# Performance work log

Measured on AMD Instinct MI355X. Metric: run time of the kernel, lower is better.

## Reference

```python
import jax, jax.numpy as jnp
import numpy as np

HID = 256
IN_DIM = 256
OUT_DIM = 10
L_CYCLES = 6
H_CYCLES = 3
BATCH = 131072
LN_EPS = 1e-5


def _layernorm(v, w, b):
    mu = jnp.mean(v, axis=-1, keepdims=True)
    var = jnp.mean(jnp.square(v - mu), axis=-1, keepdims=True)
    return (v - mu) * jax.lax.rsqrt(var + LN_EPS) * w + b


def setup_inputs() -> dict:
    key = jax.random.key(0)
    ks = jax.random.split(key, 12)
    s = lambda fan_in: 1.0 / np.sqrt(fan_in)
    inp = {
        "x": jax.random.normal(ks[0], (BATCH, IN_DIM), dtype=jnp.float32),
        "W_in": jax.random.uniform(ks[1], (IN_DIM, HID), jnp.float32, -s(IN_DIM), s(IN_DIM)),
        "b_in": jnp.zeros((HID,), jnp.float32),
        "y_init": jax.random.normal(ks[2], (1, HID), dtype=jnp.float32) * 0.02,
        "W_up": jax.random.uniform(ks[3], (HID, 4 * HID), jnp.float32, -s(HID), s(HID)),
        "b_up": jnp.zeros((4 * HID,), jnp.float32),
        "W_down": jax.random.uniform(ks[4], (4 * HID, HID), jnp.float32, -s(4 * HID), s(4 * HID)),
        "b_down": jnp.zeros((HID,), jnp.float32),
        "ln_w": jnp.ones((HID,), jnp.float32),
        "ln_b": jnp.zeros((HID,), jnp.float32),
        "W_comb": jax.random.uniform(ks[5], (2 * HID, HID), jnp.float32, -s(2 * HID), s(2 * HID)),
        "b_comb": jnp.zeros((HID,), jnp.float32),
        "W_yt": jax.random.uniform(ks[6], (HID, HID), jnp.float32, -s(HID), s(HID)),
        "b_yt": jnp.zeros((HID,), jnp.float32),
        "W_head": jax.random.uniform(ks[7], (HID, OUT_DIM), jnp.float32, -s(HID), s(HID)),
        "b_head": jnp.zeros((OUT_DIM,), jnp.float32),
    }
    return inp


def reference(x, W_in, b_in, y_init, W_up, b_up, W_down, b_down, ln_w, ln_b,
              W_comb, b_comb, W_yt, b_yt, W_head, b_head):
    z = x @ W_in + b_in                      # [B, H]
    y = jnp.broadcast_to(y_init, (x.shape[0], HID))
    for _ in range(H_CYCLES):
        for _ in range(L_CYCLES):
            h = jax.nn.gelu(z @ W_up + b_up, approximate=False)
            h = h @ W_down + b_down
            z = _layernorm(z + h, ln_w, ln_b)
        combined = jnp.concatenate([z, y], axis=-1)   # [B, 2H]
        h = jax.nn.gelu(combined @ W_comb + b_comb, approximate=False)
        y = y + h @ W_yt + b_yt
    return y @ W_head + b_head
```

## Files before the change

### kernel.cpp

```cpp
#include <hip/hip_runtime.h>

typedef _Float16 h16;
typedef h16 h16x8 __attribute__((ext_vector_type(8)));
typedef float f32x4 __attribute__((ext_vector_type(4)));

#define MFMA16(a, b, c) __builtin_amdgcn_mfma_f32_16x16x32_f16(a, b, c, 0, 0, 0)

typedef __attribute__((address_space(1))) const char gconst_char;
typedef __attribute__((address_space(3))) char lds_char;
#define GL_LDS16(g, l) __builtin_amdgcn_global_load_lds((gconst_char*)(g), (lds_char*)(l), 16, 0, 0)

#define WIN_CSH   16384
#define WIN_OFF   0
#define WUP_CSH   16384
#define WUP_OFF   131072
#define WDN_CSH   16384
#define WDN_OFF   655360
#define WCOMB_CSH 32768
#define WCOMB_OFF 1179648
#define WYT_CSH   16384
#define WYT_OFF   1441792
#define WHEAD_SZ  8192
#define WHEAD_OFF 1572864
#define ZY_OFF    1581056
#define ZY_BYTES  (131072UL * 512UL * 2UL)

#define L_WUP0 0
#define L_WUP1 16384
#define L_WDN0 32768
#define L_WDN1 49152
#define L_HS   65536
#define L_BUP  76288
#define L_BDN  80384
#define L_LNW  81408
#define L_LNB  82432
#define SMEM_MEGA 83456

#define C_WC0 0
#define C_WC1 32768
#define C_WY0 65536
#define C_WY1 81920
#define C_GS  98304
#define C_BC  109056
#define C_BY  110080
#define SMEM_COMB 111104

#define SMEM_HEAD 8192

#define SLICE_W 42

__device__ __forceinline__ void stage_calls(const char* src, char* dst, int calls, int wave,
                                            int nw, int lane) {
  for (int i = wave; i < calls; i += nw)
    GL_LDS16(src + i * 1024 + lane * 16, dst + i * 1024);
}

__device__ __forceinline__ float gelu_f(float x) {
  float t = x * (1.5957691216f + 0.0713548354f * x * x);
  float e = __expf(-t);
  return x * __builtin_amdgcn_rcpf(1.0f + e);
}

__global__ void prepC_kernel(const float* __restrict__ src, h16* __restrict__ dst,
                             int Nsrc, int CSHh, int tot) {
  for (int d = blockIdx.x * 256 + threadIdx.x; d < tot; d += gridDim.x * 256) {
    int chunk = d / CSHh, r = d % CSHh;
    int frag = r >> 9, lane = (r >> 3) & 63, j = r & 7;
    int kk = frag >> 1, nt = frag & 1, q = lane >> 4, c = lane & 15;
    int k = kk * 32 + q * 8 + j;
    int n = chunk * 32 + nt * 16 + c;
    dst[d] = (h16)src[(long)k * Nsrc + n];
  }
}
__global__ void prepD_kernel(const float* __restrict__ src, h16* __restrict__ dst, int tot) {
  for (int d = blockIdx.x * 256 + threadIdx.x; d < tot; d += gridDim.x * 256) {
    int chunk = d >> 13, r = d & 8191;
    int nt = r >> 9, lane = (r >> 3) & 63, j = r & 7;
    int q = lane >> 4, c = lane & 15;
    int k = chunk * 32 + q * 8 + j;
    dst[d] = (h16)src[(long)k * 256 + nt * 16 + c];
  }
}
__global__ void prepH_kernel(const float* __restrict__ src, h16* __restrict__ dst) {
  for (int d = blockIdx.x * 256 + threadIdx.x; d < 4096; d += gridDim.x * 256) {
    int kk = d >> 9, lane = (d >> 3) & 63, j = d & 7;
    int q = lane >> 4, c = lane & 15;
    int k = kk * 32 + q * 8 + j;
    dst[d] = (h16)((c < 10) ? src[k * 10 + c] : 0.0f);
  }
}

__global__ __launch_bounds__(512, 2) void mega_kernel(
    const float* x, h16* zy,
    const char* __restrict__ winP, const char* __restrict__ wupP, const char* __restrict__ wdnP,
    const float* __restrict__ b_in, const float* __restrict__ b_up,
    const float* __restrict__ b_down, const float* __restrict__ ln_w,
    const float* __restrict__ ln_b, const float* __restrict__ y_init, int first) {
  extern __shared__ char smem[];
  const int tid = threadIdx.x, wave = tid >> 6, lane = tid & 63;
  const int q = lane >> 4, c = lane & 15;
  const int lane16 = lane << 4;
  const long m0 = (long)blockIdx.x * 128 + wave * 16;

  float* bupL = (float*)(smem + L_BUP);
  float* bdnL = (float*)(smem + L_BDN);
  float* lnwL = (float*)(smem + L_LNW);
  float* lnbL = (float*)(smem + L_LNB);
  for (int i = tid; i < 1024; i += 512) bupL[i] = b_up[i];
  if (tid < 256) { bdnL[tid] = b_down[tid]; lnwL[tid] = ln_w[tid]; lnbL[tid] = ln_b[tid]; }

  f32x4 acc2[16];
  h16x8 az[8];
  h16* sl = (h16*)(smem + L_HS + wave * (SLICE_W * 16 * 2));
  const f32x4 vzero = {0.0f, 0.0f, 0.0f, 0.0f};

  if (first) {
#pragma unroll
    for (int kk = 0; kk < 8; ++kk) {
      const float* p = x + (m0 + c) * 256 + kk * 32 + q * 8;
      f32x4 u0 = *(const f32x4*)p;
      f32x4 u1 = *(const f32x4*)(p + 4);
      h16x8 a;
      a[0] = (h16)u0[0]; a[1] = (h16)u0[1]; a[2] = (h16)u0[2]; a[3] = (h16)u0[3];
      a[4] = (h16)u1[0]; a[5] = (h16)u1[1]; a[6] = (h16)u1[2]; a[7] = (h16)u1[3];
      az[kk] = a;
    }
#pragma unroll
    for (int nt = 0; nt < 16; ++nt) acc2[nt] = vzero;

    stage_calls(winP, smem + L_WUP0, 16, wave, 8, lane);
    __syncthreads();
#pragma unroll
    for (int ncI = 0; ncI < 8; ++ncI) {
      if (ncI < 7)
        stage_calls(winP + (ncI + 1) * WIN_CSH, smem + (((ncI + 1) & 1) ? L_WUP1 : L_WUP0),
                    16, wave, 8, lane);
      const char* wb = smem + ((ncI & 1) ? L_WUP1 : L_WUP0);
#pragma unroll
      for (int kk = 0; kk < 8; ++kk)
#pragma unroll
        for (int nt = 0; nt < 2; ++nt) {
          h16x8 b = *(const h16x8*)(wb + ((kk * 2 + nt) << 10) + lane16);
          acc2[ncI * 2 + nt] = MFMA16(az[kk], b, acc2[ncI * 2 + nt]);
        }
      __syncthreads();
    }
#pragma unroll
    for (int nt = 0; nt < 16; ++nt) {
      float bi = b_in[nt * 16 + c];
#pragma unroll
      for (int r = 0; r < 4; ++r) acc2[nt][r] += bi;
    }
#pragma unroll
    for (int kk = 0; kk < 8; ++kk) {
      const float* p = y_init + kk * 32 + q * 8;
      f32x4 u0 = *(const f32x4*)p;
      f32x4 u1 = *(const f32x4*)(p + 4);
      h16x8 a;
      a[0] = (h16)u0[0]; a[1] = (h16)u0[1]; a[2] = (h16)u0[2]; a[3] = (h16)u0[3];
      a[4] = (h16)u1[0]; a[5] = (h16)u1[1]; a[6] = (h16)u1[2]; a[7] = (h16)u1[3];
      *(h16x8*)(zy + (m0 + c) * 512 + 256 + kk * 32 + q * 8) = a;
    }
    stage_calls(wupP, smem + L_WUP0, 16, wave, 8, lane);
    stage_calls(wdnP, smem + L_WDN0, 16, wave, 8, lane);
#pragma unroll
    for (int kk = 0; kk < 8; ++kk) {
#pragma unroll
      for (int n2 = 0; n2 < 2; ++n2)
#pragma unroll
        for (int r = 0; r < 4; ++r)
          sl[(q * 4 + r) * SLICE_W + n2 * 16 + c] = (h16)acc2[kk * 2 + n2][r];
      az[kk] = *(const h16x8*)(sl + c * SLICE_W + q * 8);
    }
  } else {
    stage_calls(wupP, smem + L_WUP0, 16, wave, 8, lane);
    stage_calls(wdnP, smem + L_WDN0, 16, wave, 8, lane);
#pragma unroll
    for (int kk = 0; kk < 8; ++kk)
      az[kk] = *(const h16x8*)(zy + (m0 + c) * 512 + kk * 32 + q * 8);
#pragma unroll
    for (int kk = 0; kk < 8; ++kk) {
      *(h16x8*)(sl + c * SLICE_W + q * 8) = az[kk];
#pragma unroll
      for (int n2 = 0; n2 < 2; ++n2)
#pragma unroll
        for (int r = 0; r < 4; ++r)
          acc2[kk * 2 + n2][r] = (float)sl[(q * 4 + r) * SLICE_W + n2 * 16 + c];
    }
  }

  for (int it = 0; it < 6; ++it) {
    for (int nc = 0; nc < 32; ++nc) {
      const int tc = it * 32 + nc;
      __syncthreads();
      if (tc < 191) {
        const int nxt = (nc + 1) & 31;
        char* wu = smem + (((tc + 1) & 1) ? L_WUP1 : L_WUP0);
        char* wd = smem + (((tc + 1) & 1) ? L_WDN1 : L_WDN0);
        stage_calls(wupP + nxt * WUP_CSH, wu, 16, wave, 8, lane);
        stage_calls(wdnP + nxt * WDN_CSH, wd, 16, wave, 8, lane);
      }
      const char* wub = smem + ((tc & 1) ? L_WUP1 : L_WUP0);
      const char* wdb = smem + ((tc & 1) ? L_WDN1 : L_WDN0);

      f32x4 acc1[2];
      acc1[0] = vzero; acc1[1] = vzero;
#pragma unroll
      for (int kk = 0; kk < 8; ++kk)
#pragma unroll
        for (int nt = 0; nt < 2; ++nt) {
          h16x8 b = *(const h16x8*)(wub + ((kk * 2 + nt) << 10) + lane16);
          acc1[nt] = MFMA16(az[kk], b, acc1[nt]);
        }
#pragma unroll
      for (int nt = 0; nt < 2; ++nt) {
        float bu = bupL[nc * 32 + nt * 16 + c];
#pragma unroll
        for (int r = 0; r < 4; ++r) {
          float g = gelu_f(acc1[nt][r] + bu);
          sl[(q * 4 + r) * SLICE_W + nt * 16 + c] = (h16)g;
        }
      }
      h16x8 ah = *(const h16x8*)(sl + c * SLICE_W + q * 8);
#pragma unroll
      for (int nt = 0; nt < 16; ++nt) {
        h16x8 b = *(const h16x8*)(wdb + (nt << 10) + lane16);
        acc2[nt] = MFMA16(ah, b, acc2[nt]);
      }
    }

    {
      float sum[4] = {0, 0, 0, 0}, sq[4] = {0, 0, 0, 0};
#pragma unroll
      for (int nt = 0; nt < 16; ++nt) {
        float bd = bdnL[nt * 16 + c];
#pragma unroll
        for (int r = 0; r < 4; ++r) {
          float v = acc2[nt][r] + bd;
          acc2[nt][r] = v;
          sum[r] += v;
          sq[r] += v * v;
        }
      }
#pragma unroll
      for (int r = 0; r < 4; ++r)
#pragma unroll
        for (int m = 1; m < 16; m <<= 1) {
          sum[r] += __shfl_xor(sum[r], m, 16);
          sq[r] += __shfl_xor(sq[r], m, 16);
        }
#pragma unroll
      for (int r = 0; r < 4; ++r) {
        float mu = sum[r] * (1.0f / 256.0f);
        float var = sq[r] * (1.0f / 256.0f) - mu * mu;
        float rs = __builtin_amdgcn_rsqf(var + 1e-5f);
        sum[r] = mu; sq[r] = rs;
      }
#pragma unroll
      for (int nt = 0; nt < 16; ++nt) {
        float w = lnwL[nt * 16 + c], bb = lnbL[nt * 16 + c];
#pragma unroll
        for (int r = 0; r < 4; ++r)
          acc2[nt][r] = (acc2[nt][r] - sum[r]) * sq[r] * w + bb;
      }
    }
    if (it < 5) {
#pragma unroll
      for (int kk = 0; kk < 8; ++kk) {
#pragma unroll
        for (int n2 = 0; n2 < 2; ++n2)
#pragma unroll
          for (int r = 0; r < 4; ++r)
            sl[(q * 4 + r) * SLICE_W + n2 * 16 + c] = (h16)acc2[kk * 2 + n2][r];
        az[kk] = *(const h16x8*)(sl + c * SLICE_W + q * 8);
      }
    }
  }

#pragma unroll
  for (int kk = 0; kk < 8; ++kk) {
#pragma unroll
    for (int n2 = 0; n2 < 2; ++n2)
#pragma unroll
      for (int r = 0; r < 4; ++r)
        sl[(q * 4 + r) * SLICE_W + n2 * 16 + c] = (h16)acc2[kk * 2 + n2][r];
    *(h16x8*)(zy + (m0 + c) * 512 + kk * 32 + q * 8) =
        *(const h16x8*)(sl + c * SLICE_W + q * 8);
  }
}

__global__ __launch_bounds__(512, 2) void comb_kernel(
    h16* zy, const char* __restrict__ wcP, const char* __restrict__ wytP,
    const float* __restrict__ b_comb, const float* __restrict__ b_yt,
    const float* __restrict__ y_init, int first) {
  extern __shared__ char smem[];
  const int tid = threadIdx.x, wave = tid >> 6, lane = tid & 63;
  const int q = lane >> 4, c = lane & 15;
  const int lane16 = lane << 4;
  const long m0 = (long)blockIdx.x * 128 + wave * 16;

  float* bcL = (float*)(smem + C_BC);
  float* byL = (float*)(smem + C_BY);
  if (tid < 256) { bcL[tid] = b_comb[tid]; byL[tid] = b_yt[tid]; }

  h16* sl = (h16*)(smem + C_GS + wave * (SLICE_W * 16 * 2));
  const f32x4 vzero = {0.0f, 0.0f, 0.0f, 0.0f};

  stage_calls(wcP, smem + C_WC0, 32, wave, 8, lane);
  stage_calls(wytP, smem + C_WY0, 16, wave, 8, lane);

  h16x8 a[16];
#pragma unroll
  for (int kk = 0; kk < 16; ++kk)
    a[kk] = *(const h16x8*)(zy + (m0 + c) * 512 + kk * 32 + q * 8);

  f32x4 acc2[16];
  if (first) {
#pragma unroll
    for (int nt = 0; nt < 16; ++nt) {
      float yv = y_init[nt * 16 + c];
#pragma unroll
      for (int r = 0; r < 4; ++r) acc2[nt][r] = yv;
    }
  } else {
#pragma unroll
    for (int kk = 0; kk < 8; ++kk) {
      *(h16x8*)(sl + c * SLICE_W + q * 8) = a[8 + kk];
#pragma unroll
      for (int n2 = 0; n2 < 2; ++n2)
#pragma unroll
        for (int r = 0; r < 4; ++r)
          acc2[kk * 2 + n2][r] = (float)sl[(q * 4 + r) * SLICE_W + n2 * 16 + c];
    }
  }

  for (int nc = 0; nc < 8; ++nc) {
    __syncthreads();
    if (nc < 7) {
      int nb = (nc + 1) & 1;
      stage_calls(wcP + (nc + 1) * WCOMB_CSH, smem + (nb ? C_WC1 : C_WC0), 32, wave, 8, lane);
      stage_calls(wytP + (nc + 1) * WYT_CSH, smem + (nb ? C_WY1 : C_WY0), 16, wave, 8, lane);
    }
    const char* wcb = smem + ((nc & 1) ? C_WC1 : C_WC0);
    const char* wyb = smem + ((nc & 1) ? C_WY1 : C_WY0);

    f32x4 acc1[2];
    acc1[0] = vzero; acc1[1] = vzero;
#pragma unroll
    for (int kk = 0; kk < 16; ++kk)
#pragma unroll
      for (int nt = 0; nt < 2; ++nt) {
        h16x8 b = *(const h16x8*)(wcb + ((kk * 2 + nt) << 10) + lane16);
        acc1[nt] = MFMA16(a[kk], b, acc1[nt]);
      }
#pragma unroll
    for (int nt = 0; nt < 2; ++nt) {
      float bc = bcL[nc * 32 + nt * 16 + c];
#pragma unroll
      for (int r = 0; r < 4; ++r) {
        float g = gelu_f(acc1[nt][r] + bc);
        sl[(q * 4 + r) * SLICE_W + nt * 16 + c] = (h16)g;
      }
    }
    h16x8 ah = *(const h16x8*)(sl + c * SLICE_W + q * 8);
#pragma unroll
    for (int nt = 0; nt < 16; ++nt) {
      h16x8 b = *(const h16x8*)(wyb + (nt << 10) + lane16);
      acc2[nt] = MFMA16(ah, b, acc2[nt]);
    }
  }

#pragma unroll
  for (int kk = 0; kk < 8; ++kk) {
#pragma unroll
    for (int n2 = 0; n2 < 2; ++n2) {
      float by = byL[(kk * 2 + n2) * 16 + c];
#pragma unroll
      for (int r = 0; r < 4; ++r)
        sl[(q * 4 + r) * SLICE_W + n2 * 16 + c] = (h16)(acc2[kk * 2 + n2][r] + by);
    }
    *(h16x8*)(zy + (m0 + c) * 512 + 256 + kk * 32 + q * 8) =
        *(const h16x8*)(sl + c * SLICE_W + q * 8);
  }
}

__global__ __launch_bounds__(256) void head_kernel(const h16* zy, const char* __restrict__ whP,
                                                   const float* __restrict__ b_head,
                                                   float* __restrict__ out) {
  extern __shared__ char smem[];
  const int tid = threadIdx.x, wave = tid >> 6, lane = tid & 63;
  const int q = lane >> 4, c = lane & 15;
  const int lane16 = lane << 4;
  const long m0 = (long)blockIdx.x * 128 + wave * 32;

  stage_calls(whP, smem, 8, wave, 4, lane);
  __syncthreads();

  f32x4 acc[2];
  const f32x4 vzero = {0.0f, 0.0f, 0.0f, 0.0f};
  acc[0] = vzero; acc[1] = vzero;
#pragma unroll
  for (int kk = 0; kk < 8; ++kk) {
    h16x8 b = *(const h16x8*)(smem + (kk << 10) + lane16);
#pragma unroll
    for (int rt = 0; rt < 2; ++rt) {
      h16x8 a = *(const h16x8*)(zy + (m0 + rt * 16 + c) * 512 + 256 + kk * 32 + q * 8);
      acc[rt] = MFMA16(a, b, acc[rt]);
    }
  }
  if (c < 10) {
    float bh = b_head[c];
#pragma unroll
    for (int rt = 0; rt < 2; ++rt)
#pragma unroll
      for (int r = 0; r < 4; ++r)
        out[(m0 + rt * 16 + q * 4 + r) * 10 + c] = acc[rt][r] + bh;
  }
}

extern "C" void kernel_launch(void* const* d_in, const int* in_sizes, int n_in, void* d_out,
                              int out_size, void* d_ws, size_t ws_size, hipStream_t stream) {
  (void)in_sizes; (void)n_in; (void)out_size;
  const float* x      = (const float*)d_in[0];
  const float* W_in   = (const float*)d_in[1];
  const float* b_in   = (const float*)d_in[2];
  const float* y_init = (const float*)d_in[3];
  const float* W_up   = (const float*)d_in[4];
  const float* b_up   = (const float*)d_in[5];
  const float* W_down = (const float*)d_in[6];
  const float* b_down = (const float*)d_in[7];
  const float* ln_w   = (const float*)d_in[8];
  const float* ln_b   = (const float*)d_in[9];
  const float* W_comb = (const float*)d_in[10];
  const float* b_comb = (const float*)d_in[11];
  const float* W_yt   = (const float*)d_in[12];
  const float* b_yt   = (const float*)d_in[13];
  const float* W_head = (const float*)d_in[14];
  const float* b_head = (const float*)d_in[15];

  char* ws = (char*)d_ws;
  h16* winP   = (h16*)(ws + WIN_OFF);
  h16* wupP   = (h16*)(ws + WUP_OFF);
  h16* wdnP   = (h16*)(ws + WDN_OFF);
  h16* wcombP = (h16*)(ws + WCOMB_OFF);
  h16* wytP   = (h16*)(ws + WYT_OFF);
  h16* wheadP = (h16*)(ws + WHEAD_OFF);
  h16* zy = (ws_size >= (size_t)ZY_OFF + ZY_BYTES) ? (h16*)(ws + ZY_OFF) : (h16*)d_in[0];

  hipFuncSetAttribute((const void*)mega_kernel, hipFuncAttributeMaxDynamicSharedMemorySize,
                      SMEM_MEGA);
  hipFuncSetAttribute((const void*)comb_kernel, hipFuncAttributeMaxDynamicSharedMemorySize,
                      SMEM_COMB);

  {
    int tot;
    tot = 8 * (WIN_CSH / 2);
    prepC_kernel<<<dim3((tot + 255) / 256), dim3(256), 0, stream>>>(W_in, winP, 256, WIN_CSH / 2, tot);
    tot = 32 * (WUP_CSH / 2);
    prepC_kernel<<<dim3((tot + 255) / 256), dim3(256), 0, stream>>>(W_up, wupP, 1024, WUP_CSH / 2, tot);
    tot = 8 * (WCOMB_CSH / 2);
    prepC_kernel<<<dim3((tot + 255) / 256), dim3(256), 0, stream>>>(W_comb, wcombP, 256, WCOMB_CSH / 2, tot);
    tot = 32 * (WDN_CSH / 2);
    prepD_kernel<<<dim3((tot + 255) / 256), dim3(256), 0, stream>>>(W_down, wdnP, tot);
    tot = 8 * (WYT_CSH / 2);
    prepD_kernel<<<dim3((tot + 255) / 256), dim3(256), 0, stream>>>(W_yt, wytP, tot);
    prepH_kernel<<<dim3(16), dim3(256), 0, stream>>>(W_head, wheadP);
  }

  for (int h = 0; h < 3; ++h) {
    mega_kernel<<<dim3(1024), dim3(512), SMEM_MEGA, stream>>>(
        x, zy, (const char*)winP, (const char*)wupP, (const char*)wdnP, b_in, b_up, b_down,
        ln_w, ln_b, y_init, (h == 0) ? 1 : 0);
    comb_kernel<<<dim3(1024), dim3(512), SMEM_COMB, stream>>>(
        zy, (const char*)wcombP, (const char*)wytP, b_comb, b_yt, y_init, (h == 0) ? 1 : 0);
  }
  head_kernel<<<dim3(1024), dim3(256), SMEM_HEAD, stream>>>(zy, (const char*)wheadP, b_head,
                                                            (float*)d_out);
}
```

Measured before the change: 4.618 ms.

## Process 32 rows per wave in mega_kernel to reuse staged weight fragments

Each wave now handles two 16-row tiles (256 rows per block, half as many blocks), so every B fragment read from LDS feeds two MFMAs instead of one. The goal is to halve LDS weight-read traffic and global weight restaging per row through the 192-chunk up/down MLP loop. In exchange it doubles accumulator registers (two 16x f32x4 sets), which with launch_bounds(512,2) risks spills or lower occupancy, and it enlarges the LDS slice area.

Result: faster. 4.143 ms (-10.3%).

```diff
diff --git a/kernel.cpp b/kernel.cpp
--- a/kernel.cpp
+++ b/kernel.cpp
@@ -30,11 +30,11 @@
 #define L_WDN0 32768
 #define L_WDN1 49152
 #define L_HS   65536
-#define L_BUP  76288
-#define L_BDN  80384
-#define L_LNW  81408
-#define L_LNB  82432
-#define SMEM_MEGA 83456
+#define L_BUP  87040
+#define L_BDN  91136
+#define L_LNW  92160
+#define L_LNB  93184
+#define SMEM_MEGA 94208
 
 #define C_WC0 0
 #define C_WC1 32768
@@ -100,7 +100,7 @@
   const int tid = threadIdx.x, wave = tid >> 6, lane = tid & 63;
   const int q = lane >> 4, c = lane & 15;
   const int lane16 = lane << 4;
-  const long m0 = (long)blockIdx.x * 128 + wave * 16;
+  const long m0 = (long)blockIdx.x * 256 + wave * 32;
 
   float* bupL = (float*)(smem + L_BUP);
   float* bdnL = (float*)(smem + L_BDN);
@@ -109,24 +109,30 @@
   for (int i = tid; i < 1024; i += 512) bupL[i] = b_up[i];
   if (tid < 256) { bdnL[tid] = b_down[tid]; lnwL[tid] = ln_w[tid]; lnbL[tid] = ln_b[tid]; }
 
-  f32x4 acc2[16];
-  h16x8 az[8];
-  h16* sl = (h16*)(smem + L_HS + wave * (SLICE_W * 16 * 2));
+  f32x4 acc2a[16], acc2b[16];
+  h16x8 aza[8], azb[8];
+  h16* sl = (h16*)(smem + L_HS + wave * (32 * SLICE_W * 2));
   const f32x4 vzero = {0.0f, 0.0f, 0.0f, 0.0f};
 
   if (first) {
 #pragma unroll
     for (int kk = 0; kk < 8; ++kk) {
-      const float* p = x + (m0 + c) * 256 + kk * 32 + q * 8;
-      f32x4 u0 = *(const f32x4*)p;
-      f32x4 u1 = *(const f32x4*)(p + 4);
+      const float* pa = x + (m0 + c) * 256 + kk * 32 + q * 8;
+      f32x4 u0 = *(const f32x4*)pa;
+      f32x4 u1 = *(const f32x4*)(pa + 4);
       h16x8 a;
       a[0] = (h16)u0[0]; a[1] = (h16)u0[1]; a[2] = (h16)u0[2]; a[3] = (h16)u0[3];
       a[4] = (h16)u1[0]; a[5] = (h16)u1[1]; a[6] = (h16)u1[2]; a[7] = (h16)u1[3];
-      az[kk] = a;
-    }
-#pragma unroll
-    for (int nt = 0; nt < 16; ++nt) acc2[nt] = vzero;
+      aza[kk] = a;
+      const float* pb = x + (m0 + 16 + c) * 256 + kk * 32 + q * 8;
+      u0 = *(const f32x4*)pb;
+      u1 = *(const f32x4*)(pb + 4);
+      a[0] = (h16)u0[0]; a[1] = (h16)u0[1]; a[2] = (h16)u0[2]; a[3] = (h16)u0[3];
+      a[4] = (h16)u1[0]; a[5] = (h16)u1[1]; a[6] = (h16)u1[2]; a[7] = (h16)u1[3];
+      azb[kk] = a;
+    }
+#pragma unroll
+    for (int nt = 0; nt < 16; ++nt) { acc2a[nt] = vzero; acc2b[nt] = vzero; }
 
     stage_calls(winP, smem + L_WUP0, 16, wave, 8, lane);
     __syncthreads();
@@ -141,7 +147,8 @@
 #pragma unroll
         for (int nt = 0; nt < 2; ++nt) {
           h16x8 b = *(const h16x8*)(wb + ((kk * 2 + nt) << 10) + lane16);
-          acc2[ncI * 2 + nt] = MFMA16(az[kk], b, acc2[ncI * 2 + nt]);
+          acc2a[ncI * 2 + nt] = MFMA16(aza[kk], b, acc2a[ncI * 2 + nt]);
+          acc2b[ncI * 2 + nt] = MFMA16(azb[kk], b, acc2b[ncI * 2 + nt]);
         }
       __syncthreads();
     }
@@ -149,7 +156,7 @@
     for (int nt = 0; nt < 16; ++nt) {
       float bi = b_in[nt * 16 + c];
 #pragma unroll
-      for (int r = 0; r < 4; ++r) acc2[nt][r] += bi;
+      for (int r = 0; r < 4; ++r) { acc2a[nt][r] += bi; acc2b[nt][r] += bi; }
     }
 #pragma unroll
     for (int kk = 0; kk < 8; ++kk) {
@@ -160,6 +167,7 @@
       a[0] = (h16)u0[0]; a[1] = (h16)u0[1]; a[2] = (h16)u0[2]; a[3] = (h16)u0[3];
       a[4] = (h16)u1[0]; a[5] = (h16)u1[1]; a[6] = (h16)u1[2]; a[7] = (h16)u1[3];
       *(h16x8*)(zy + (m0 + c) * 512 + 256 + kk * 32 + q * 8) = a;
+      *(h16x8*)(zy + (m0 + 16 + c) * 512 + 256 + kk * 32 + q * 8) = a;
     }
     stage_calls(wupP, smem + L_WUP0, 16, wave, 8, lane);
     stage_calls(wdnP, smem + L_WDN0, 16, wave, 8, lane);
@@ -169,23 +177,43 @@
       for (int n2 = 0; n2 < 2; ++n2)
 #pragma unroll
         for (int r = 0; r < 4; ++r)
-          sl[(q * 4 + r) * SLICE_W + n2 * 16 + c] = (h16)acc2[kk * 2 + n2][r];
-      az[kk] = *(const h16x8*)(sl + c * SLICE_W + q * 8);
+          sl[(q * 4 + r) * SLICE_W + n2 * 16 + c] = (h16)acc2a[kk * 2 + n2][r];
+      aza[kk] = *(const h16x8*)(sl + c * SLICE_W + q * 8);
+    }
+#pragma unroll
+    for (int kk = 0; kk < 8; ++kk) {
+#pragma unroll
+      for (int n2 = 0; n2 < 2; ++n2)
+#pragma unroll
+        for (int r = 0; r < 4; ++r)
+          sl[(16 + q * 4 + r) * SLICE_W + n2 * 16 + c] = (h16)acc2b[kk * 2 + n2][r];
+      azb[kk] = *(const h16x8*)(sl + (16 + c) * SLICE_W + q * 8);
     }
   } else {
     stage_calls(wupP, smem + L_WUP0, 16, wave, 8, lane);
     stage_calls(wdnP, smem + L_WDN0, 16, wave, 8, lane);
 #pragma unroll
-    for (int kk = 0; kk < 8; ++kk)
-      az[kk] = *(const h16x8*)(zy + (m0 + c) * 512 + kk * 32 + q * 8);
-#pragma unroll
-    for (int kk = 0; kk < 8; ++kk) {
-      *(h16x8*)(sl + c * SLICE_W + q * 8) = az[kk];
+    for (int kk = 0; kk < 8; ++kk) {
+      aza[kk] = *(const h16x8*)(zy + (m0 + c) * 512 + kk * 32 + q * 8);
+      azb[kk] = *(const h16x8*)(zy + (m0 + 16 + c) * 512 + kk * 32 + q * 8);
+    }
+#pragma unroll
+    for (int kk = 0; kk < 8; ++kk) {
+      *(h16x8*)(sl + c * SLICE_W + q * 8) = aza[kk];
 #pragma unroll
       for (int n2 = 0; n2 < 2; ++n2)
 #pragma unroll
         for (int r = 0; r < 4; ++r)
-          acc2[kk * 2 + n2][r] = (float)sl[(q * 4 + r) * SLICE_W + n2 * 16 + c];
+          acc2a[kk * 2 + n2][r] = (float)sl[(q * 4 + r) * SLICE_W + n2 * 16 + c];
+    }
+#pragma unroll
+    for (int kk = 0; kk < 8; ++kk) {
+      *(h16x8*)(sl + (16 + c) * SLICE_W + q * 8) = azb[kk];
+#pragma unroll
+      for (int n2 = 0; n2 < 2; ++n2)
+#pragma unroll
+        for (int r = 0; r < 4; ++r)
+          acc2b[kk * 2 + n2][r] = (float)sl[(16 + q * 4 + r) * SLICE_W + n2 * 16 + c];
     }
   }
 
@@ -203,29 +231,34 @@
       const char* wub = smem + ((tc & 1) ? L_WUP1 : L_WUP0);
       const char* wdb = smem + ((tc & 1) ? L_WDN1 : L_WDN0);
 
-      f32x4 acc1[2];
-      acc1[0] = vzero; acc1[1] = vzero;
-#pragma unroll
-      for (int kk = 0; kk < 8; ++kk)
-#pragma unroll
-        for (int nt = 0; nt < 2; ++nt) {
-          h16x8 b = *(const h16x8*)(wub + ((kk * 2 + nt) << 10) + lane16);
-          acc1[nt] = MFMA16(az[kk], b, acc1[nt]);
+      f32x4 acc1a0 = vzero, acc1a1 = vzero, acc1b0 = vzero, acc1b1 = vzero;
+#pragma unroll
+      for (int kk = 0; kk < 8; ++kk) {
+        h16x8 b0 = *(const h16x8*)(wub + ((kk * 2 + 0) << 10) + lane16);
+        acc1a0 = MFMA16(aza[kk], b0, acc1a0);
+        acc1b0 = MFMA16(azb[kk], b0, acc1b0);
+        h16x8 b1 = *(const h16x8*)(wub + ((kk * 2 + 1) << 10) + lane16);
+        acc1a1 = MFMA16(aza[kk], b1, acc1a1);
+        acc1b1 = MFMA16(azb[kk], b1, acc1b1);
+      }
+      {
+        float bu0 = bupL[nc * 32 + c];
+        float bu1 = bupL[nc * 32 + 16 + c];
+#pragma unroll
+        for (int r = 0; r < 4; ++r) {
+          sl[(q * 4 + r) * SLICE_W + c] = (h16)gelu_f(acc1a0[r] + bu0);
+          sl[(q * 4 + r) * SLICE_W + 16 + c] = (h16)gelu_f(acc1a1[r] + bu1);
+          sl[(16 + q * 4 + r) * SLICE_W + c] = (h16)gelu_f(acc1b0[r] + bu0);
+          sl[(16 + q * 4 + r) * SLICE_W + 16 + c] = (h16)gelu_f(acc1b1[r] + bu1);
         }
-#pragma unroll
-      for (int nt = 0; nt < 2; ++nt) {
-        float bu = bupL[nc * 32 + nt * 16 + c];
-#pragma unroll
-        for (int r = 0; r < 4; ++r) {
-          float g = gelu_f(acc1[nt][r] + bu);
-          sl[(q * 4 + r) * SLICE_W + nt * 16 + c] = (h16)g;
-        }
-      }
-      h16x8 ah = *(const h16x8*)(sl + c * SLICE_W + q * 8);
+      }
+      h16x8 ah0 = *(const h16x8*)(sl + c * SLICE_W + q * 8);
+      h16x8 ah1 = *(const h16x8*)(sl + (16 + c) * SLICE_W + q * 8);
 #pragma unroll
       for (int nt = 0; nt < 16; ++nt) {
         h16x8 b = *(const h16x8*)(wdb + (nt << 10) + lane16);
-        acc2[nt] = MFMA16(ah, b, acc2[nt]);
+        acc2a[nt] = MFMA16(ah0, b, acc2a[nt]);
+        acc2b[nt] = MFMA16(ah1, b, acc2b[nt]);
       }
     }
 
@@ -236,8 +269,8 @@
         float bd = bdnL[nt * 16 + c];
 #pragma unroll
         for (int r = 0; r < 4; ++r) {
-          float v = acc2[nt][r] + bd;
-          acc2[nt][r] = v;
+          float v = acc2a[nt][r] + bd;
+          acc2a[nt][r] = v;
           sum[r] += v;
           sq[r] += v * v;
         }
@@ -261,7 +294,42 @@
         float w = lnwL[nt * 16 + c], bb = lnbL[nt * 16 + c];
 #pragma unroll
         for (int r = 0; r < 4; ++r)
-          acc2[nt][r] = (acc2[nt][r] - sum[r]) * sq[r] * w + bb;
+          acc2a[nt][r] = (acc2a[nt][r] - sum[r]) * sq[r] * w + bb;
+      }
+    }
+    {
+      float sum[4] = {0, 0, 0, 0}, sq[4] = {0, 0, 0, 0};
+#pragma unroll
+      for (int nt = 0; nt < 16; ++nt) {
+        float bd = bdnL[nt * 16 + c];
+#pragma unroll
+        for (int r = 0; r < 4; ++r) {
+          float v = acc2b[nt][r] + bd;
+          acc2b[nt][r] = v;
+          sum[r] += v;
+          sq[r] += v * v;
+        }
+      }
+#pragma unroll
+      for (int r = 0; r < 4; ++r)
+#pragma unroll
+        for (int m = 1; m < 16; m <<= 1) {
+          sum[r] += __shfl_xor(sum[r], m, 16);
+          sq[r] += __shfl_xor(sq[r], m, 16);
+        }
+#pragma unroll
+      for (int r = 0; r < 4; ++r) {
+        float mu = sum[r] * (1.0f / 256.0f);
+        float var = sq[r] * (1.0f / 256.0f) - mu * mu;
+        float rs = __builtin_amdgcn_rsqf(var + 1e-5f);
+        sum[r] = mu; sq[r] = rs;
+      }
+#pragma unroll
+      for (int nt = 0; nt < 16; ++nt) {
+        float w = lnwL[nt * 16 + c], bb = lnbL[nt * 16 + c];
+#pragma unroll
+        for (int r = 0; r < 4; ++r)
+          acc2b[nt][r] = (acc2b[nt][r] - sum[r]) * sq[r] * w + bb;
       }
     }
     if (it < 5) {
@@ -271,8 +339,17 @@
         for (int n2 = 0; n2 < 2; ++n2)
 #pragma unroll
           for (int r = 0; r < 4; ++r)
-            sl[(q * 4 + r) * SLICE_W + n2 * 16 + c] = (h16)acc2[kk * 2 + n2][r];
-        az[kk] = *(const h16x8*)(sl + c * SLICE_W + q * 8);
+            sl[(q * 4 + r) * SLICE_W + n2 * 16 + c] = (h16)acc2a[kk * 2 + n2][r];
+        aza[kk] = *(const h16x8*)(sl + c * SLICE_W + q * 8);
+      }
+#pragma unroll
+      for (int kk = 0; kk < 8; ++kk) {
+#pragma unroll
+        for (int n2 = 0; n2 < 2; ++n2)
+#pragma unroll
+          for (int r = 0; r < 4; ++r)
+            sl[(16 + q * 4 + r) * SLICE_W + n2 * 16 + c] = (h16)acc2b[kk * 2 + n2][r];
+        azb[kk] = *(const h16x8*)(sl + (16 + c) * SLICE_W + q * 8);
       }
     }
   }
@@ -283,9 +360,19 @@
     for (int n2 = 0; n2 < 2; ++n2)
 #pragma unroll
       for (int r = 0; r < 4; ++r)
-        sl[(q * 4 + r) * SLICE_W + n2 * 16 + c] = (h16)acc2[kk * 2 + n2][r];
+        sl[(q * 4 + r) * SLICE_W + n2 * 16 + c] = (h16)acc2a[kk * 2 + n2][r];
     *(h16x8*)(zy + (m0 + c) * 512 + kk * 32 + q * 8) =
         *(const h16x8*)(sl + c * SLICE_W + q * 8);
+  }
+#pragma unroll
+  for (int kk = 0; kk < 8; ++kk) {
+#pragma unroll
+    for (int n2 = 0; n2 < 2; ++n2)
+#pragma unroll
+      for (int r = 0; r < 4; ++r)
+        sl[(16 + q * 4 + r) * SLICE_W + n2 * 16 + c] = (h16)acc2b[kk * 2 + n2][r];
+    *(h16x8*)(zy + (m0 + 16 + c) * 512 + kk * 32 + q * 8) =
+        *(const h16x8*)(sl + (16 + c) * SLICE_W + q * 8);
   }
 }
 
@@ -468,7 +555,7 @@
   }
 
   for (int h = 0; h < 3; ++h) {
-    mega_kernel<<<dim3(1024), dim3(512), SMEM_MEGA, stream>>>(
+    mega_kernel<<<dim3(512), dim3(512), SMEM_MEGA, stream>>>(
         x, zy, (const char*)winP, (const char*)wupP, (const char*)wdnP, b_in, b_up, b_down,
         ln_w, ln_b, y_init, (h == 0) ? 1 : 0);
     comb_kernel<<<dim3(1024), dim3(512), SMEM_COMB, stream>>>(
```
